# Optimization experiments

Hardware: AMD Instinct MI355X
Metric: run time of the kernel (lower is better)

The kernel has to match this reference:

```python
import jax, jax.numpy as jnp
import numpy as np
from jax import lax

D_MODEL = 1024
N_EXPERTS = 8
N_ACTIVE = 2
FFN_HIDDEN = int(D_MODEL * 2.0)


def setup_inputs() -> dict:
    key = jax.random.key(0)
    ks = jax.random.split(key, 7)
    B, T = 2, 2048
    s_in = 1.0 / np.sqrt(D_MODEL)
    s_h = 1.0 / np.sqrt(FFN_HIDDEN)
    return {
        "x": jax.random.normal(ks[0], (B, T, D_MODEL), dtype=jnp.float32),
        # router: torch Linear(d_model, n_experts, bias=False) weight [E, D]
        "router_w": jax.random.uniform(ks[1], (N_EXPERTS, D_MODEL), jnp.float32, -s_in, s_in),
        # stacked expert FFN params: w1 [E, H, D], b1 [E, H], w2 [E, D, H], b2 [E, D]
        "w1": jax.random.uniform(ks[2], (N_EXPERTS, FFN_HIDDEN, D_MODEL), jnp.float32, -s_in, s_in),
        "b1": jax.random.uniform(ks[3], (N_EXPERTS, FFN_HIDDEN), jnp.float32, -s_in, s_in),
        "w2": jax.random.uniform(ks[4], (N_EXPERTS, D_MODEL, FFN_HIDDEN), jnp.float32, -s_h, s_h),
        "b2": jax.random.uniform(ks[5], (N_EXPERTS, D_MODEL), jnp.float32, -s_h, s_h),
    }


def reference(x, router_w, w1, b1, w2, b2):
    B, T, D = x.shape
    N = B * T
    xf = x.reshape(N, D)

    logits = xf @ router_w.T                      # [N, E]
    probs = jax.nn.softmax(logits, axis=-1)       # [N, E]

    # --- aux load-balancing loss (f_i is non-differentiable, from indices) ---
    _, disp_idx = lax.top_k(logits, N_ACTIVE)     # [N, K]
    disp_mask = jax.nn.one_hot(disp_idx, N_EXPERTS, dtype=logits.dtype).sum(axis=1)  # [N, E]
    f_i = disp_mask.sum(axis=0) / (N * N_ACTIVE)  # [E]
    P_i = probs.mean(axis=0)                      # [E]
    aux_loss = N_EXPERTS * jnp.sum(f_i * P_i)

    # --- top-k combine weights, renormalized ---
    topk_w, topk_idx = lax.top_k(probs, N_ACTIVE)                 # [N, K]
    topk_w = topk_w / topk_w.sum(axis=-1, keepdims=True)
    # scatter top-k weights into dense [N, E] combine matrix (zeros elsewhere)
    combine_w = (jax.nn.one_hot(topk_idx, N_EXPERTS, dtype=xf.dtype) * topk_w[..., None]).sum(axis=1)

    # --- expert FFNs, weighted combine (loop over small fixed expert set) ---
    out = jnp.zeros_like(xf)
    for e in range(N_EXPERTS):
        h = jax.nn.silu(xf @ w1[e].T + b1[e])     # [N, H]
        y = h @ w2[e].T + b2[e]                   # [N, D]
        out = out + combine_w[:, e:e + 1] * y

    return out.reshape(B, T, D), aux_loss
```

## Files before the change

kernel.cpp:

```cpp
#include <hip/hip_runtime.h>
#include <cstdint>
#include <cstddef>

#define D_MODEL 1024
#define N_EXPERTS 8
#define FFN_H 2048
#define N_TOK 4096
#define CAP 2048

typedef float f32x4 __attribute__((ext_vector_type(4)));
typedef __bf16 bf16x8 __attribute__((ext_vector_type(8)));

static constexpr size_t XB_OFF   = 0;
static constexpr size_t W1B_OFF  = XB_OFF  + (size_t)N_TOK * D_MODEL * 2;
static constexpr size_t W2B_OFF  = W1B_OFF + (size_t)N_EXPERTS * FFN_H * D_MODEL * 2;
static constexpr size_t HBUF_OFF = W2B_OFF + (size_t)N_EXPERTS * D_MODEL * FFN_H * 2;
static constexpr size_t YBUF_OFF = HBUF_OFF + (size_t)N_EXPERTS * CAP * FFN_H * 2;
static constexpr size_t CNT_OFF  = YBUF_OFF + (size_t)N_EXPERTS * CAP * D_MODEL * 2;
static constexpr size_t PSUM_OFF = CNT_OFF + 32;
static constexpr size_t TOK_OFF  = PSUM_OFF + 32;
static constexpr size_t TIX_OFF  = TOK_OFF + (size_t)N_EXPERTS * CAP * 4;
static constexpr size_t TIW_OFF  = TIX_OFF + (size_t)N_TOK * 8;

__device__ __forceinline__ void async_ld16(const void* g, void* l) {
    __builtin_amdgcn_global_load_lds(
        (const __attribute__((address_space(1))) unsigned int*)g,
        (__attribute__((address_space(3))) unsigned int*)l, 16, 0, 0);
}

__global__ __launch_bounds__(256) void prep_kernel(const float* __restrict__ x,
                                                   const float* __restrict__ rw,
                                                   const float* __restrict__ w1,
                                                   const float* __restrict__ w2,
                                                   __bf16* __restrict__ xb,
                                                   __bf16* __restrict__ w1b,
                                                   __bf16* __restrict__ w2b,
                                                   int* __restrict__ counts,
                                                   float* __restrict__ psum,
                                                   int* __restrict__ tok_list,
                                                   int2* __restrict__ tinfo_idx,
                                                   float2* __restrict__ tinfo_w) {
    __shared__ float rws[N_EXPERTS * D_MODEL];
    __shared__ int s_e0[64], s_e1[64], s_r0[64], s_r1[64];
    __shared__ float s_w0[64], s_w1[64];
    __shared__ int hist[8], base[8];
    __shared__ float pacc[8];

    int tid = threadIdx.x;
    int b = blockIdx.x;
    if (b >= 64) {
        int c = b - 64;
        const float* src; __bf16* dst; size_t bb;
        if (c < 8192) { src = w1; dst = w1b; bb = (size_t)c * 2048; }
        else          { src = w2; dst = w2b; bb = (size_t)(c - 8192) * 2048; }
        size_t i = bb + (size_t)tid * 8;
        float4 a = *reinterpret_cast<const float4*>(src + i);
        float4 d = *reinterpret_cast<const float4*>(src + i + 4);
        bf16x8 r;
        r[0] = (__bf16)a.x; r[1] = (__bf16)a.y; r[2] = (__bf16)a.z; r[3] = (__bf16)a.w;
        r[4] = (__bf16)d.x; r[5] = (__bf16)d.y; r[6] = (__bf16)d.z; r[7] = (__bf16)d.w;
        *reinterpret_cast<bf16x8*>(dst + i) = r;
        return;
    }

    {
        size_t base_i = (size_t)b * 64 * D_MODEL;
        for (int i = tid; i < 64 * D_MODEL / 8; i += 256) {
            size_t off = base_i + (size_t)i * 8;
            float4 a = *reinterpret_cast<const float4*>(x + off);
            float4 d = *reinterpret_cast<const float4*>(x + off + 4);
            bf16x8 r;
            r[0] = (__bf16)a.x; r[1] = (__bf16)a.y; r[2] = (__bf16)a.z; r[3] = (__bf16)a.w;
            r[4] = (__bf16)d.x; r[5] = (__bf16)d.y; r[6] = (__bf16)d.z; r[7] = (__bf16)d.w;
            *reinterpret_cast<bf16x8*>(xb + off) = r;
        }
    }
    for (int i = tid * 4; i < N_EXPERTS * D_MODEL; i += 256 * 4)
        *reinterpret_cast<float4*>(&rws[i]) = *reinterpret_cast<const float4*>(&rw[i]);
    if (tid < 8) { hist[tid] = 0; pacc[tid] = 0.f; }
    __syncthreads();

    int wave = tid >> 6, lane = tid & 63;
    float psacc[8] = {};
    for (int it = 0; it < 16; ++it) {
        int li = wave * 16 + it;
        int t = b * 64 + li;
        const float* xr = x + (size_t)t * D_MODEL;
        float acc[8] = {};
#pragma unroll
        for (int i = 0; i < D_MODEL / 64; ++i) {
            float xv = xr[lane + 64 * i];
#pragma unroll
            for (int e = 0; e < 8; ++e) acc[e] += xv * rws[e * D_MODEL + lane + 64 * i];
        }
        float logit[8];
#pragma unroll
        for (int e = 0; e < 8; ++e) {
            float v = acc[e];
            for (int off = 32; off; off >>= 1) v += __shfl_xor(v, off);
            logit[e] = v;
        }
        float mx = logit[0];
#pragma unroll
        for (int e = 1; e < 8; ++e) mx = fmaxf(mx, logit[e]);
        float p[8], s = 0.f;
#pragma unroll
        for (int e = 0; e < 8; ++e) { p[e] = expf(logit[e] - mx); s += p[e]; }
        float inv = 1.f / s;
#pragma unroll
        for (int e = 0; e < 8; ++e) { p[e] *= inv; psacc[e] += p[e]; }
        int e0 = 0; float p0 = p[0];
#pragma unroll
        for (int e = 1; e < 8; ++e) if (p[e] > p0) { p0 = p[e]; e0 = e; }
        int e1 = -1; float p1 = -1.f;
#pragma unroll
        for (int e = 0; e < 8; ++e) if (e != e0 && p[e] > p1) { p1 = p[e]; e1 = e; }
        float invw = 1.f / (p0 + p1);
        if (lane == 0) {
            s_e0[li] = e0; s_e1[li] = e1;
            s_w0[li] = p0 * invw; s_w1[li] = p1 * invw;
        }
    }
    if (lane == 0)
#pragma unroll
        for (int e = 0; e < 8; ++e) atomicAdd(&pacc[e], psacc[e]);
    __syncthreads();

    if (tid < 64) {
        s_r0[tid] = atomicAdd(&hist[s_e0[tid]], 1);
        s_r1[tid] = atomicAdd(&hist[s_e1[tid]], 1);
    }
    __syncthreads();
    if (tid < 8) {
        base[tid] = atomicAdd(&counts[tid], hist[tid]);
        atomicAdd(&psum[tid], pacc[tid]);
    }
    __syncthreads();
    if (tid < 64) {
        int t = b * 64 + tid;
        int e0 = s_e0[tid], e1 = s_e1[tid];
        int q0 = min(base[e0] + s_r0[tid], CAP - 1);
        int q1 = min(base[e1] + s_r1[tid], CAP - 1);
        tok_list[e0 * CAP + q0] = t;
        tok_list[e1 * CAP + q1] = t;
        tinfo_idx[t] = make_int2(e0 * CAP + q0, e1 * CAP + q1);
        tinfo_w[t] = make_float2(s_w0[tid], s_w1[tid]);
    }
}

template <int KDIM, bool PASS2>
__global__ __launch_bounds__(256) void ffn_kernel(const __bf16* __restrict__ A_base,
                                                  const __bf16* __restrict__ B_base,
                                                  const float* __restrict__ bias,
                                                  const int* __restrict__ counts,
                                                  const int* __restrict__ tok_list,
                                                  __bf16* __restrict__ Out_base) {
    constexpr int BROWS = PASS2 ? D_MODEL : FFN_H;
    constexpr int OSTRIDE = PASS2 ? D_MODEL : FFN_H;
    constexpr int NT = BROWS / 128;
    constexpr int CSTR = 136;
    int bid = blockIdx.x;
    int e = bid & 7;
    int r = bid >> 3;
    int n0 = (r % NT) * 128;
    int m0 = (r / NT) * 128;
    int cnt = min(counts[e], CAP);
    if (m0 >= cnt) return;

    __shared__ __bf16 s_buf[64 * CSTR];
    __shared__ int s_tok[128];

    int tid = threadIdx.x;
    if (!PASS2 && tid < 128) {
        int slot = min(m0 + tid, cnt - 1);
        s_tok[tid] = tok_list[e * CAP + slot];
    }
    __syncthreads();

    int colk = (tid & 3) * 8;
    const __bf16 *a_src0, *a_src1;
    if (PASS2) {
        int s0 = min(m0 + (tid >> 2), cnt - 1);
        int s1 = min(m0 + 64 + (tid >> 2), cnt - 1);
        a_src0 = A_base + ((size_t)e * CAP + s0) * KDIM + colk;
        a_src1 = A_base + ((size_t)e * CAP + s1) * KDIM + colk;
    } else {
        a_src0 = A_base + (size_t)s_tok[tid >> 2] * KDIM + colk;
        a_src1 = A_base + (size_t)s_tok[64 + (tid >> 2)] * KDIM + colk;
    }
    const __bf16* b_src0 = B_base + ((size_t)e * BROWS + n0 + (tid >> 2)) * KDIM + colk;
    const __bf16* b_src1 = b_src0 + (size_t)64 * KDIM;

    char* lds_a = (char*)s_buf + (tid >> 6) * 1024;
    char* lds_b = (char*)s_buf + 8192 + (tid >> 6) * 1024;

    int wv = tid >> 6, lane = tid & 63;
    int wm = wv >> 1, wn = wv & 1;
    int lm = lane & 15, q = lane >> 4;
    int a_base = (wm * 64 + lm) * 32 + q * 8;
    int b_base = 4096 + (wn * 64 + lm) * 32 + q * 8;

    f32x4 acc[4][4] = {};
    for (int k0 = 0; k0 < KDIM; k0 += 32) {
        async_ld16(a_src0 + k0, lds_a);
        async_ld16(a_src1 + k0, lds_a + 4096);
        async_ld16(b_src0 + k0, lds_b);
        async_ld16(b_src1 + k0, lds_b + 4096);
        __syncthreads();
        bf16x8 af[4], bf[4];
#pragma unroll
        for (int f = 0; f < 4; ++f) {
            af[f] = *reinterpret_cast<const bf16x8*>(&s_buf[a_base + f * 16 * 32]);
            bf[f] = *reinterpret_cast<const bf16x8*>(&s_buf[b_base + f * 16 * 32]);
        }
#pragma unroll
        for (int fm = 0; fm < 4; ++fm)
#pragma unroll
            for (int fn = 0; fn < 4; ++fn)
                acc[fm][fn] = __builtin_amdgcn_mfma_f32_16x16x32_bf16(af[fm], bf[fn], acc[fm][fn], 0, 0, 0);
        __syncthreads();
    }

#pragma unroll
    for (int h = 0; h < 2; ++h) {
        if (wm == h) {
#pragma unroll
            for (int fn = 0; fn < 4; ++fn) {
                int col = wn * 64 + fn * 16 + lm;
                float bv = bias[e * BROWS + n0 + col];
#pragma unroll
                for (int fm = 0; fm < 4; ++fm) {
                    int rloc = fm * 16 + q * 4;
#pragma unroll
                    for (int i = 0; i < 4; ++i) {
                        float v = acc[fm][fn][i] + bv;
                        if (!PASS2) v = v / (1.f + __expf(-v));
                        s_buf[(rloc + i) * CSTR + col] = (__bf16)v;
                    }
                }
            }
        }
        __syncthreads();
#pragma unroll
        for (int j = 0; j < 4; ++j) {
            int rloc = (tid >> 4) + j * 16;
            int coloff = (tid & 15) * 8;
            int slot = m0 + h * 64 + rloc;
            if (slot < cnt) {
                bf16x8 vv = *reinterpret_cast<const bf16x8*>(&s_buf[rloc * CSTR + coloff]);
                *reinterpret_cast<bf16x8*>(
                    Out_base + ((size_t)e * CAP + slot) * OSTRIDE + n0 + coloff) = vv;
            }
        }
        __syncthreads();
    }
}

__global__ __launch_bounds__(256) void combine_kernel(const __bf16* __restrict__ ybuf,
                                                      const int2* __restrict__ tinfo_idx,
                                                      const float2* __restrict__ tinfo_w,
                                                      const int* __restrict__ counts,
                                                      const float* __restrict__ psum,
                                                      float* __restrict__ out) {
    int tid = threadIdx.x;
    if (blockIdx.x == 0 && tid == 0) {
        float s = 0.f;
#pragma unroll
        for (int e = 0; e < 8; ++e)
            s += ((float)counts[e] / (float)(N_TOK * 2)) * (psum[e] / (float)N_TOK);
        out[(size_t)N_TOK * D_MODEL] = 8.f * s;
    }
    int t = blockIdx.x * 2 + (tid >> 7);
    int d0 = (tid & 127) * 8;
    int2 ix = tinfo_idx[t];
    float2 w = tinfo_w[t];
    bf16x8 ya = *reinterpret_cast<const bf16x8*>(ybuf + (size_t)ix.x * D_MODEL + d0);
    bf16x8 yb = *reinterpret_cast<const bf16x8*>(ybuf + (size_t)ix.y * D_MODEL + d0);
    float4 o0, o1;
    o0.x = w.x * (float)ya[0] + w.y * (float)yb[0];
    o0.y = w.x * (float)ya[1] + w.y * (float)yb[1];
    o0.z = w.x * (float)ya[2] + w.y * (float)yb[2];
    o0.w = w.x * (float)ya[3] + w.y * (float)yb[3];
    o1.x = w.x * (float)ya[4] + w.y * (float)yb[4];
    o1.y = w.x * (float)ya[5] + w.y * (float)yb[5];
    o1.z = w.x * (float)ya[6] + w.y * (float)yb[6];
    o1.w = w.x * (float)ya[7] + w.y * (float)yb[7];
    float* op = out + (size_t)t * D_MODEL + d0;
    *reinterpret_cast<float4*>(op) = o0;
    *reinterpret_cast<float4*>(op + 4) = o1;
}

extern "C" void kernel_launch(void* const* d_in, const int* in_sizes, int n_in,
                              void* d_out, int out_size, void* d_ws, size_t ws_size,
                              hipStream_t stream) {
    const float* x  = (const float*)d_in[0];
    const float* rw = (const float*)d_in[1];
    const float* w1 = (const float*)d_in[2];
    const float* b1 = (const float*)d_in[3];
    const float* w2 = (const float*)d_in[4];
    const float* b2 = (const float*)d_in[5];
    float* out = (float*)d_out;

    char* ws = (char*)d_ws;
    __bf16* xb     = (__bf16*)(ws + XB_OFF);
    __bf16* w1b    = (__bf16*)(ws + W1B_OFF);
    __bf16* w2b    = (__bf16*)(ws + W2B_OFF);
    __bf16* hbuf   = (__bf16*)(ws + HBUF_OFF);
    __bf16* ybuf   = (__bf16*)(ws + YBUF_OFF);
    int*    counts = (int*)(ws + CNT_OFF);
    float*  psum   = (float*)(ws + PSUM_OFF);
    int*    tok    = (int*)(ws + TOK_OFF);
    int2*   tix    = (int2*)(ws + TIX_OFF);
    float2* tiw    = (float2*)(ws + TIW_OFF);

    hipMemsetAsync(ws + CNT_OFF, 0, 64, stream);

    prep_kernel<<<64 + 16384, 256, 0, stream>>>(x, rw, w1, w2, xb, w1b, w2b,
                                                counts, psum, tok, tix, tiw);

    ffn_kernel<D_MODEL, false><<<8 * (FFN_H / 128) * (CAP / 128), 256, 0, stream>>>(
        xb, w1b, b1, counts, tok, hbuf);
    ffn_kernel<FFN_H, true><<<8 * (D_MODEL / 128) * (CAP / 128), 256, 0, stream>>>(
        hbuf, w2b, b2, counts, tok, ybuf);

    combine_kernel<<<N_TOK / 2, 256, 0, stream>>>(ybuf, tix, tiw, counts, psum, out);
}
```

Before: 324.1 us.

## Use 512-thread FFN blocks: wider N tile for pass 1, split-K for pass 2

Both expert FFN GEMM kernels now launch 512-thread blocks. Pass 1 uses a 128x256 tile so each A (token) load is reused across twice as many output columns. Pass 2 splits K=2048 into two halves handled by separate wave groups, which are reduced through LDS. The LDS-staged coalesced epilogue is replaced with direct scalar bf16 global stores, which may cost store efficiency and adds extra barriers for the split-K reduction.

```diff
diff --git a/kernel.cpp b/kernel.cpp
--- a/kernel.cpp
+++ b/kernel.cpp
@@ -149,25 +149,26 @@
 }
 
 template <int KDIM, bool PASS2>
-__global__ __launch_bounds__(256) void ffn_kernel(const __bf16* __restrict__ A_base,
+__global__ __launch_bounds__(512) void ffn_kernel(const __bf16* __restrict__ A_base,
                                                   const __bf16* __restrict__ B_base,
                                                   const float* __restrict__ bias,
                                                   const int* __restrict__ counts,
                                                   const int* __restrict__ tok_list,
                                                   __bf16* __restrict__ Out_base) {
+    constexpr int BN = PASS2 ? 128 : 256;
     constexpr int BROWS = PASS2 ? D_MODEL : FFN_H;
-    constexpr int OSTRIDE = PASS2 ? D_MODEL : FFN_H;
-    constexpr int NT = BROWS / 128;
-    constexpr int CSTR = 136;
+    constexpr int KR = 1024;
+    constexpr int SB0 = PASS2 ? 8192 : 4096;
+
     int bid = blockIdx.x;
     int e = bid & 7;
     int r = bid >> 3;
-    int n0 = (r % NT) * 128;
-    int m0 = (r / NT) * 128;
+    int n0 = (r & 7) * BN;
+    int m0 = (r >> 3) * 128;
     int cnt = min(counts[e], CAP);
     if (m0 >= cnt) return;
 
-    __shared__ __bf16 s_buf[64 * CSTR];
+    __shared__ __bf16 s_buf[16384];
     __shared__ int s_tok[128];
 
     int tid = threadIdx.x;
@@ -178,40 +179,48 @@
     __syncthreads();
 
     int colk = (tid & 3) * 8;
-    const __bf16 *a_src0, *a_src1;
+    int rrow = tid >> 2;
+    const __bf16 *a_src, *b_src, *b_src2 = nullptr;
     if (PASS2) {
-        int s0 = min(m0 + (tid >> 2), cnt - 1);
-        int s1 = min(m0 + 64 + (tid >> 2), cnt - 1);
-        a_src0 = A_base + ((size_t)e * CAP + s0) * KDIM + colk;
-        a_src1 = A_base + ((size_t)e * CAP + s1) * KDIM + colk;
+        int slot = min(m0 + rrow, cnt - 1);
+        a_src = A_base + ((size_t)e * CAP + slot) * KDIM + colk;
     } else {
-        a_src0 = A_base + (size_t)s_tok[tid >> 2] * KDIM + colk;
-        a_src1 = A_base + (size_t)s_tok[64 + (tid >> 2)] * KDIM + colk;
-    }
-    const __bf16* b_src0 = B_base + ((size_t)e * BROWS + n0 + (tid >> 2)) * KDIM + colk;
-    const __bf16* b_src1 = b_src0 + (size_t)64 * KDIM;
-
-    char* lds_a = (char*)s_buf + (tid >> 6) * 1024;
-    char* lds_b = (char*)s_buf + 8192 + (tid >> 6) * 1024;
+        a_src = A_base + (size_t)s_tok[rrow] * KDIM + colk;
+    }
+    b_src = B_base + ((size_t)e * BROWS + n0 + rrow) * KDIM + colk;
+    if (!PASS2) b_src2 = b_src + (size_t)128 * KDIM;
 
     int wv = tid >> 6, lane = tid & 63;
-    int wm = wv >> 1, wn = wv & 1;
+    int g  = PASS2 ? (wv >> 2) : 0;
+    int wl = PASS2 ? (wv & 3) : wv;
+    int wm = PASS2 ? (wl >> 1) : (wl >> 2);
+    int wn = PASS2 ? (wl & 1) : (wl & 3);
     int lm = lane & 15, q = lane >> 4;
-    int a_base = (wm * 64 + lm) * 32 + q * 8;
-    int b_base = 4096 + (wn * 64 + lm) * 32 + q * 8;
+
+    char* ldsA = (char*)s_buf + wv * 1024;
+    char* ldsB = (char*)s_buf + SB0 * 2 + wv * 1024;
+
+    int a_off = g * 4096 + (wm * 64 + lm) * 32 + q * 8;
+    int b_off = SB0 + (PASS2 ? g * 4096 : 0) + (wn * 64 + lm) * 32 + q * 8;
 
     f32x4 acc[4][4] = {};
-    for (int k0 = 0; k0 < KDIM; k0 += 32) {
-        async_ld16(a_src0 + k0, lds_a);
-        async_ld16(a_src1 + k0, lds_a + 4096);
-        async_ld16(b_src0 + k0, lds_b);
-        async_ld16(b_src1 + k0, lds_b + 4096);
+    for (int k0 = 0; k0 < KR; k0 += 32) {
+        if (PASS2) {
+            async_ld16(a_src + k0,      ldsA);
+            async_ld16(a_src + KR + k0, ldsA + 8192);
+            async_ld16(b_src + k0,      ldsB);
+            async_ld16(b_src + KR + k0, ldsB + 8192);
+        } else {
+            async_ld16(a_src + k0,  ldsA);
+            async_ld16(b_src + k0,  ldsB);
+            async_ld16(b_src2 + k0, ldsB + 8192);
+        }
         __syncthreads();
         bf16x8 af[4], bf[4];
 #pragma unroll
         for (int f = 0; f < 4; ++f) {
-            af[f] = *reinterpret_cast<const bf16x8*>(&s_buf[a_base + f * 16 * 32]);
-            bf[f] = *reinterpret_cast<const bf16x8*>(&s_buf[b_base + f * 16 * 32]);
+            af[f] = *reinterpret_cast<const bf16x8*>(&s_buf[a_off + f * 16 * 32]);
+            bf[f] = *reinterpret_cast<const bf16x8*>(&s_buf[b_off + f * 16 * 32]);
         }
 #pragma unroll
         for (int fm = 0; fm < 4; ++fm)
@@ -221,38 +230,50 @@
         __syncthreads();
     }
 
-#pragma unroll
-    for (int h = 0; h < 2; ++h) {
-        if (wm == h) {
-#pragma unroll
-            for (int fn = 0; fn < 4; ++fn) {
-                int col = wn * 64 + fn * 16 + lm;
-                float bv = bias[e * BROWS + n0 + col];
-#pragma unroll
-                for (int fm = 0; fm < 4; ++fm) {
-                    int rloc = fm * 16 + q * 4;
-#pragma unroll
-                    for (int i = 0; i < 4; ++i) {
+    if (PASS2) {
+        float* red = (float*)s_buf;
+#pragma unroll
+        for (int fm = 0; fm < 4; ++fm) {
+            if (g == 1) {
+                float* dst = red + wl * 1024 + lane * 16;
+#pragma unroll
+                for (int fn = 0; fn < 4; ++fn)
+                    *reinterpret_cast<f32x4*>(dst + fn * 4) = acc[fm][fn];
+            }
+            __syncthreads();
+            if (g == 0) {
+                const float* srcp = red + wl * 1024 + lane * 16;
+#pragma unroll
+                for (int fn = 0; fn < 4; ++fn)
+                    acc[fm][fn] += *reinterpret_cast<const f32x4*>(srcp + fn * 4);
+            }
+            __syncthreads();
+        }
+    }
+
+    if (!PASS2 || g == 0) {
+#pragma unroll
+        for (int fn = 0; fn < 4; ++fn) {
+            int n = n0 + wn * 64 + fn * 16 + lm;
+            float bv = bias[e * BROWS + n];
+#pragma unroll
+            for (int fm = 0; fm < 4; ++fm) {
+                int rbase = wm * 64 + fm * 16 + q * 4;
+#pragma unroll
+                for (int i = 0; i < 4; ++i) {
+                    int slot = m0 + rbase + i;
+                    if (slot < cnt) {
                         float v = acc[fm][fn][i] + bv;
-                        if (!PASS2) v = v / (1.f + __expf(-v));
-                        s_buf[(rloc + i) * CSTR + col] = (__bf16)v;
+                        if (!PASS2) {
+                            float sv = v / (1.f + __expf(-v));
+                            Out_base[((size_t)e * CAP + slot) * FFN_H + n] = (__bf16)sv;
+                        } else {
+                            Out_base[((size_t)e * CAP + slot) * D_MODEL + n] = (__bf16)v;
+                        }
                     }
                 }
             }
         }
-        __syncthreads();
-#pragma unroll
-        for (int j = 0; j < 4; ++j) {
-            int rloc = (tid >> 4) + j * 16;
-            int coloff = (tid & 15) * 8;
-            int slot = m0 + h * 64 + rloc;
-            if (slot < cnt) {
-                bf16x8 vv = *reinterpret_cast<const bf16x8*>(&s_buf[rloc * CSTR + coloff]);
-                *reinterpret_cast<bf16x8*>(
-                    Out_base + ((size_t)e * CAP + slot) * OSTRIDE + n0 + coloff) = vv;
-            }
-        }
-        __syncthreads();
     }
 }
 
@@ -318,9 +339,9 @@
     prep_kernel<<<64 + 16384, 256, 0, stream>>>(x, rw, w1, w2, xb, w1b, w2b,
                                                 counts, psum, tok, tix, tiw);
 
-    ffn_kernel<D_MODEL, false><<<8 * (FFN_H / 128) * (CAP / 128), 256, 0, stream>>>(
+    ffn_kernel<D_MODEL, false><<<8 * 8 * (CAP / 128), 512, 0, stream>>>(
         xb, w1b, b1, counts, tok, hbuf);
-    ffn_kernel<FFN_H, true><<<8 * (D_MODEL / 128) * (CAP / 128), 256, 0, stream>>>(
+    ffn_kernel<FFN_H, true><<<8 * 8 * (CAP / 128), 512, 0, stream>>>(
         hbuf, w2b, b2, counts, tok, ybuf);
 
     combine_kernel<<<N_TOK / 2, 256, 0, stream>>>(ybuf, tix, tiw, counts, psum, out);
```

New measurement: 357.0 us. +10.2%, slower.
